# Optimization experiments

Hardware: AMD Instinct MI355X
Metric: run time of the kernel (lower is better)

Reference implementation:

```python
import jax, jax.numpy as jnp
import numpy as np

D_MODEL = 1024
N_HEADS = 16
D_K = D_MODEL // N_HEADS
ROPE_THETA = 10000.0


def setup_inputs() -> dict:
    key = jax.random.key(0)
    ks = jax.random.split(key, 5)
    B, S = 2, 2048
    std = (2.0 / (D_MODEL + D_MODEL)) ** 0.5
    x = jax.random.normal(ks[0], (B, S, D_MODEL), dtype=jnp.float32)
    Wq = jax.random.normal(ks[1], (D_MODEL, D_MODEL), dtype=jnp.float32) * std
    Wk = jax.random.normal(ks[2], (D_MODEL, D_MODEL), dtype=jnp.float32) * std
    Wv = jax.random.normal(ks[3], (D_MODEL, D_MODEL), dtype=jnp.float32) * std
    Wo = jax.random.normal(ks[4], (D_MODEL, D_MODEL), dtype=jnp.float32) * std
    token_positions = jnp.arange(S, dtype=jnp.int64 if jax.config.jax_enable_x64 else jnp.int32)
    return {"x": x, "Wq": Wq, "Wk": Wk, "Wv": Wv, "Wo": Wo,
            "token_positions": token_positions}


def _apply_rope(t, token_positions):
    # t: [B, H, S, d_k]; token_positions: [S]
    inv_freq = 1.0 / (ROPE_THETA ** (jnp.arange(0, D_K, 2, dtype=jnp.float32) / D_K))  # [d_k/2]
    freqs = token_positions.astype(jnp.float32)[:, None] * inv_freq[None, :]  # [S, d_k/2]
    cos, sin = jnp.cos(freqs), jnp.sin(freqs)
    x1, x2 = t[..., ::2], t[..., 1::2]
    xr = x1 * cos - x2 * sin
    yr = x1 * sin + x2 * cos
    # interleave back to even/odd positions
    out = jnp.stack([xr, yr], axis=-1).reshape(t.shape)
    return out


def reference(x, Wq, Wk, Wv, Wo, token_positions):
    B, S, D = x.shape
    H, dk = N_HEADS, D_K
    # projections: weight is [d_out, d_in], applied as x @ W.T
    def proj_heads(W):
        y = jnp.einsum('bsd,ed->bse', x, W)
        return y.reshape(B, S, H, dk).transpose(0, 2, 1, 3)  # [B,H,S,dk]
    q = proj_heads(Wq)
    k = proj_heads(Wk)
    v = proj_heads(Wv)
    q = _apply_rope(q, token_positions)
    k = _apply_rope(k, token_positions)
    scores = jnp.einsum('bhqd,bhkd->bhqk', q, k) / jnp.sqrt(jnp.float32(dk))
    causal = jnp.tril(jnp.ones((S, S), dtype=bool))
    scores = jnp.where(causal, scores, -jnp.inf)
    attn = jax.nn.softmax(scores, axis=-1)
    out = jnp.einsum('bhqk,bhkd->bhqd', attn, v)  # [B,H,S,dk]
    out = out.transpose(0, 2, 1, 3).reshape(B, S, D)
    return jnp.einsum('bsd,ed->bse', out, Wo)
```

## Files before the change

### kernel.cpp

```cpp
#include <hip/hip_runtime.h>

typedef __bf16 bf16x8 __attribute__((ext_vector_type(8)));
typedef float f32x4 __attribute__((ext_vector_type(4)));
typedef unsigned short u16x8 __attribute__((ext_vector_type(8)));


__device__ __forceinline__ unsigned short f2bf(float f) {
  unsigned u = __builtin_bit_cast(unsigned, f);
  u = (u + 0x7FFFu + ((u >> 16) & 1u)) >> 16;
  return (unsigned short)u;
}

__device__ __forceinline__ unsigned cvt_pk_bf16(float lo, float hi) {
  unsigned r;
  asm("v_cvt_pk_bf16_f32 %0, %1, %2" : "=v"(r) : "v"(lo), "v"(hi));
  return r;
}

__device__ __forceinline__ void load_lds16(const void* g, void* l) {
  __builtin_amdgcn_global_load_lds(
      (__attribute__((address_space(1))) void*)g,
      (__attribute__((address_space(3))) void*)l, 16, 0, 0);
}

__global__ __launch_bounds__(256) void k_convert(
    const float* __restrict__ x,
    const float* __restrict__ wq, const float* __restrict__ wk,
    const float* __restrict__ wv, const float* __restrict__ wo,
    unsigned short* __restrict__ xb,
    unsigned short* __restrict__ wqb, unsigned short* __restrict__ wkb,
    unsigned short* __restrict__ wvb, unsigned short* __restrict__ wob) {
  const int g = blockIdx.x * 256 + threadIdx.x;
  const float* src;
  unsigned short* dst;
  int off;
  if (g < (1 << 20)) {
    src = x; dst = xb; off = g;
  } else {
    const int q = g - (1 << 20);
    const int t = q >> 18;
    off = q & ((1 << 18) - 1);
    src = (t == 0) ? wq : (t == 1) ? wk : (t == 2) ? wv : wo;
    dst = (t == 0) ? wqb : (t == 1) ? wkb : (t == 2) ? wvb : wob;
  }
  const float4 v = ((const float4*)src)[off];
  ushort4 r;
  r.x = f2bf(v.x); r.y = f2bf(v.y); r.z = f2bf(v.z); r.w = f2bf(v.w);
  ((ushort4*)dst)[off] = r;
}

__global__ __launch_bounds__(256) void k_rope_tab(const int* __restrict__ tpos,
                                                  float* __restrict__ ct,
                                                  float* __restrict__ st) {
  const int idx = blockIdx.x * 256 + threadIdx.x;
  const int s = idx >> 5, i = idx & 31;
  const double p = (double)tpos[s];
  const double f = p * pow(10000.0, -(double)(2 * i) / 64.0);
  ct[idx] = (float)cos(f);
  st[idx] = (float)sin(f);
}

__device__ __forceinline__ void gemm_core_1024(
    const unsigned short* __restrict__ Ag,
    const unsigned short* __restrict__ Bg,
    unsigned short* As, unsigned short* Bs, f32x4 (&acc)[4][4], int tid) {
  const int lane = tid & 63;
  const int w = tid >> 6;
  const int wm = (w >> 1) * 64;
  const int wn = (w & 1) * 64;
  const int lr = lane & 15;
  const int lg8 = (lane >> 4) * 8;
  const int c0 = tid, c1 = 256 + tid;
  const int ar0 = c0 >> 2, ac0 = (c0 & 3) * 8;
  const int ar1 = c1 >> 2, ac1 = (c1 & 3) * 8;

  auto stage = [&](int buf, int kt) {
    unsigned short* Ab = As + buf * 4096;
    unsigned short* Bb = Bs + buf * 4096;
    load_lds16(Ag + ar0 * 1024 + kt + ac0, Ab + c0 * 8);
    load_lds16(Ag + ar1 * 1024 + kt + ac1, Ab + c1 * 8);
    load_lds16(Bg + ar0 * 1024 + kt + ac0, Bb + c0 * 8);
    load_lds16(Bg + ar1 * 1024 + kt + ac1, Bb + c1 * 8);
  };

  stage(0, 0);
  stage(1, 32);
  int cur = 0;
  for (int ki = 0; ki < 32; ++ki) {
    if (ki + 2 < 32) {
      int nb = cur + 2; if (nb >= 3) nb -= 3;
      stage(nb, (ki + 2) * 32);
      asm volatile("s_waitcnt vmcnt(8)" ::: "memory");
    } else if (ki + 1 < 32) {
      asm volatile("s_waitcnt vmcnt(4)" ::: "memory");
    } else {
      asm volatile("s_waitcnt vmcnt(0)" ::: "memory");
    }
    __builtin_amdgcn_s_barrier();
    const unsigned short* Ab = As + cur * 4096;
    const unsigned short* Bb = Bs + cur * 4096;
    bf16x8 af[4], bfv[4];
#pragma unroll
    for (int mi = 0; mi < 4; ++mi)
      af[mi] = *(const bf16x8*)(Ab + (wm + mi * 16 + lr) * 32 + lg8);
#pragma unroll
    for (int ni = 0; ni < 4; ++ni)
      bfv[ni] = *(const bf16x8*)(Bb + (wn + ni * 16 + lr) * 32 + lg8);
    __builtin_amdgcn_s_setprio(1);
#pragma unroll
    for (int mi = 0; mi < 4; ++mi)
#pragma unroll
      for (int ni = 0; ni < 4; ++ni)
        acc[mi][ni] = __builtin_amdgcn_mfma_f32_16x16x32_bf16(
            af[mi], bfv[ni], acc[mi][ni], 0, 0, 0);
    __builtin_amdgcn_s_setprio(0);
    __builtin_amdgcn_s_barrier();
    ++cur; if (cur == 3) cur = 0;
  }
}

__device__ __forceinline__ void gemm_core_bm64(
    const unsigned short* __restrict__ Ag,
    const unsigned short* __restrict__ Bg,
    unsigned short* As, unsigned short* Bs, f32x4 (&acc)[2][4], int tid) {
  const int lane = tid & 63;
  const int w = tid >> 6;
  const int wm = (w >> 1) * 32;
  const int wn = (w & 1) * 64;
  const int lr = lane & 15;
  const int lg8 = (lane >> 4) * 8;
  const int ar = tid >> 2, ac = (tid & 3) * 8;
  const int c0 = tid, c1 = 256 + tid;
  const int br0 = c0 >> 2, bc0 = (c0 & 3) * 8;
  const int br1 = c1 >> 2, bc1 = (c1 & 3) * 8;

  auto stage = [&](int buf, int kt) {
    load_lds16(Ag + ar * 1024 + kt + ac, As + buf * 2048 + tid * 8);
    load_lds16(Bg + br0 * 1024 + kt + bc0, Bs + buf * 4096 + c0 * 8);
    load_lds16(Bg + br1 * 1024 + kt + bc1, Bs + buf * 4096 + c1 * 8);
  };

  stage(0, 0);
  stage(1, 32);
  int cur = 0;
  for (int ki = 0; ki < 32; ++ki) {
    if (ki + 2 < 32) {
      int nb = cur + 2; if (nb >= 3) nb -= 3;
      stage(nb, (ki + 2) * 32);
      asm volatile("s_waitcnt vmcnt(6)" ::: "memory");
    } else if (ki + 1 < 32) {
      asm volatile("s_waitcnt vmcnt(3)" ::: "memory");
    } else {
      asm volatile("s_waitcnt vmcnt(0)" ::: "memory");
    }
    __builtin_amdgcn_s_barrier();
    const unsigned short* Ab = As + cur * 2048;
    const unsigned short* Bb = Bs + cur * 4096;
    bf16x8 af[2], bfv[4];
#pragma unroll
    for (int mi = 0; mi < 2; ++mi)
      af[mi] = *(const bf16x8*)(Ab + (wm + mi * 16 + lr) * 32 + lg8);
#pragma unroll
    for (int ni = 0; ni < 4; ++ni)
      bfv[ni] = *(const bf16x8*)(Bb + (wn + ni * 16 + lr) * 32 + lg8);
    __builtin_amdgcn_s_setprio(1);
#pragma unroll
    for (int mi = 0; mi < 2; ++mi)
#pragma unroll
      for (int ni = 0; ni < 4; ++ni)
        acc[mi][ni] = __builtin_amdgcn_mfma_f32_16x16x32_bf16(
            af[mi], bfv[ni], acc[mi][ni], 0, 0, 0);
    __builtin_amdgcn_s_setprio(0);
    __builtin_amdgcn_s_barrier();
    ++cur; if (cur == 3) cur = 0;
  }
}

__global__ __launch_bounds__(256) void k_proj(
    const unsigned short* __restrict__ Xb,
    const unsigned short* __restrict__ Wq, const unsigned short* __restrict__ Wk,
    const unsigned short* __restrict__ Wv,
    const float* __restrict__ ctab, const float* __restrict__ stab,
    unsigned short* __restrict__ Qo, unsigned short* __restrict__ Ko,
    unsigned short* __restrict__ Vo) {
  __shared__ __align__(16) unsigned short As[3 * 128 * 32];
  __shared__ __align__(16) unsigned short Bs[3 * 128 * 32];
  const int z = blockIdx.z;
  const unsigned short* Wsel = (z == 0) ? Wq : (z == 1) ? Wk : Wv;
  unsigned short* Out = (z == 0) ? Qo : (z == 1) ? Ko : Vo;
  const int tid = threadIdx.x;
  const int bm = blockIdx.x * 128, bn = blockIdx.y * 128;
  f32x4 acc[4][4] = {};
  gemm_core_1024(Xb + (size_t)bm * 1024, Wsel + (size_t)bn * 1024, As, Bs, acc, tid);

  const int lane = tid & 63, w = tid >> 6;
  const int wm = (w >> 1) * 64, wn = (w & 1) * 64;
  const int lr = lane & 15, lg = lane >> 4;

  if (z == 2) {
#pragma unroll
    for (int mi = 0; mi < 4; ++mi) {
      const int r0 = bm + wm + mi * 16 + lg * 4;
      const int s = r0 & 2047, b = r0 >> 11;
#pragma unroll
      for (int ni = 0; ni < 4; ++ni) {
        const int e = bn + wn + ni * 16 + lr;
        const int h = e >> 6, d = e & 63;
        ushort4 pk;
        pk.x = f2bf(acc[mi][ni][0]);
        pk.y = f2bf(acc[mi][ni][1]);
        pk.z = f2bf(acc[mi][ni][2]);
        pk.w = f2bf(acc[mi][ni][3]);
        *(ushort4*)&Out[((size_t)(b * 16 + h) * 64 + d) * 2048 + s] = pk;
      }
    }
    return;
  }

  const bool odd = lane & 1;
#pragma unroll
  for (int mi = 0; mi < 4; ++mi) {
#pragma unroll
    for (int ni = 0; ni < 4; ++ni) {
#pragma unroll
      for (int reg = 0; reg < 4; ++reg) {
        const int r = bm + wm + mi * 16 + lg * 4 + reg;
        const int e = bn + wn + ni * 16 + lr;
        float val = acc[mi][ni][reg];
        const float partner = __shfl_xor(val, 1);
        const int s = r & 2047, b = r >> 11;
        const int h = e >> 6, d = e & 63;
        const int i = d >> 1;
        const float c = ctab[s * 32 + i];
        const float sn = stab[s * 32 + i];
        const float outv = odd ? (val * c + partner * sn) : (val * c - partner * sn);
        Out[((size_t)(b * 16 + h) * 2048 + s) * 64 + d] = f2bf(outv);
      }
    }
  }
}

__global__ __launch_bounds__(64, 2) void k_attn(
    const unsigned short* __restrict__ Q, const unsigned short* __restrict__ K,
    const unsigned short* __restrict__ Vt, unsigned short* __restrict__ O) {
  __shared__ __align__(16) unsigned short Vs[2][64 * 64];
  __shared__ __align__(16) unsigned short Pl[16 * 68];
  const int L = blockIdx.x;
  const int bh = (L & 7) * 4 + ((L >> 3) & 3);
  const int p = L >> 5;
  const int qrowA = p * 16, qrowB = (127 - p) * 16;
  const int Ta = (qrowA + 79) >> 6;
  const int Tb = (qrowB + 79) >> 6;
  const int lane = threadIdx.x & 63;
  const int lr = lane & 15, lg = lane >> 4;
  const unsigned short* Qg = Q + (size_t)bh * 2048 * 64;
  const unsigned short* Kg = K + (size_t)bh * 2048 * 64;
  const unsigned short* Vg = Vt + (size_t)bh * 64 * 2048;

  bf16x8 qfA[2], qfB[2];
#pragma unroll
  for (int h = 0; h < 2; ++h) {
    qfA[h] = *(const bf16x8*)(Qg + (qrowA + lr) * 64 + h * 32 + lg * 8);
    qfB[h] = *(const bf16x8*)(Qg + (qrowB + lr) * 64 + h * 32 + lg * 8);
  }

  u16x8 ouv;
#pragma unroll
  for (int j = 0; j < 8; ++j) ouv[j] = 0x3F80;
  const bf16x8 onesf = __builtin_bit_cast(bf16x8, ouv);

  f32x4 oA[4] = {}, oB[4] = {};
  f32x4 lAa = {}, lBa = {};
  float mA = -__builtin_inff(), mB = -__builtin_inff();

  const float SCL = 0.125f * 1.44269504088896f;

  const int kbase = lr * 64 + lg * 8;
  const int vbase = (lane >> 3) * 2048 + (((lane & 7) ^ (lane >> 3)) * 8);

  auto loadK = [&](bf16x8 (&kd)[4][2], int kv) {
    const unsigned short* base = Kg + (size_t)kv * 4096 + kbase;
#pragma unroll
    for (int nt = 0; nt < 4; ++nt)
#pragma unroll
      for (int h = 0; h < 2; ++h)
        kd[nt][h] = *(const bf16x8*)(base + nt * 1024 + h * 32);
  };
  auto issueV = [&](int buf, int kv) {
    const unsigned short* src = Vg + kv * 64 + vbase;
    unsigned short* dst = &Vs[buf][0] + lane * 8;
#pragma unroll
    for (int i0 = 0; i0 < 8; ++i0)
      load_lds16(src + i0 * 16384, dst + i0 * 512);
  };

  auto soft = [&](f32x4 (&s)[4], float& m, f32x4& la, f32x4 (&oacc)[4],
                  int qrow, bool needmask, int kv) {
    if (needmask) {
      const int qg = qrow + lr;
#pragma unroll
      for (int nt = 0; nt < 4; ++nt)
#pragma unroll
        for (int reg = 0; reg < 4; ++reg) {
          const int kg = kv * 64 + nt * 16 + lg * 4 + reg;
          if (kg > qg) s[nt][reg] = -__builtin_inff();
        }
    }
    float t0 = fmaxf(fmaxf(s[0][0], s[0][1]), fmaxf(s[0][2], s[0][3]));
    float t1 = fmaxf(fmaxf(s[1][0], s[1][1]), fmaxf(s[1][2], s[1][3]));
    float t2 = fmaxf(fmaxf(s[2][0], s[2][1]), fmaxf(s[2][2], s[2][3]));
    float t3 = fmaxf(fmaxf(s[3][0], s[3][1]), fmaxf(s[3][2], s[3][3]));
    float pm = fmaxf(fmaxf(t0, t1), fmaxf(t2, t3));
    pm = fmaxf(pm, __shfl_xor(pm, 16));
    pm = fmaxf(pm, __shfl_xor(pm, 32));
    if (__any(pm > m)) {
      const float mn = fmaxf(m, pm);
      const float al = exp2f(SCL * (m - mn));
      m = mn;
#pragma unroll
      for (int reg = 0; reg < 4; ++reg) la[reg] *= al;
#pragma unroll
      for (int nt = 0; nt < 4; ++nt)
#pragma unroll
        for (int reg = 0; reg < 4; ++reg) oacc[nt][reg] *= al;
    }
    const float msc = SCL * m;
    unsigned short* prow = Pl + lr * 68;
#pragma unroll
    for (int nt = 0; nt < 4; ++nt) {
      const float p0 = exp2f(s[nt][0] * SCL - msc);
      const float p1 = exp2f(s[nt][1] * SCL - msc);
      const float p2 = exp2f(s[nt][2] * SCL - msc);
      const float p3 = exp2f(s[nt][3] * SCL - msc);
      const unsigned w01 = cvt_pk_bf16(p0, p1);
      const unsigned w23 = cvt_pk_bf16(p2, p3);
      ushort4 pk;
      pk.x = (unsigned short)w01; pk.y = (unsigned short)(w01 >> 16);
      pk.z = (unsigned short)w23; pk.w = (unsigned short)(w23 >> 16);
      *(ushort4*)(prow + nt * 16 + lg * 4) = pk;
    }
  };

  bf16x8 kbufA[4][2], kbufB[4][2];
  loadK(kbufA, 0);
  issueV(0, 0);

  auto iter = [&](int t, bf16x8 (&kc)[4][2], bf16x8 (&kn)[4][2]) {
    const bool more = (t + 1 < Tb);
    const bool actA = (t < Ta);
    if (more) { loadK(kn, t + 1); issueV((t + 1) & 1, t + 1); }

    f32x4 sB[4], sA[4];
    __builtin_amdgcn_s_setprio(1);
#pragma unroll
    for (int nt = 0; nt < 4; ++nt) {
      f32x4 z = {0.f, 0.f, 0.f, 0.f};
      z = __builtin_amdgcn_mfma_f32_16x16x32_bf16(kc[nt][0], qfB[0], z, 0, 0, 0);
      sB[nt] = __builtin_amdgcn_mfma_f32_16x16x32_bf16(kc[nt][1], qfB[1], z, 0, 0, 0);
    }
    if (actA)
#pragma unroll
      for (int nt = 0; nt < 4; ++nt) {
        f32x4 z = {0.f, 0.f, 0.f, 0.f};
        z = __builtin_amdgcn_mfma_f32_16x16x32_bf16(kc[nt][0], qfA[0], z, 0, 0, 0);
        sA[nt] = __builtin_amdgcn_mfma_f32_16x16x32_bf16(kc[nt][1], qfA[1], z, 0, 0, 0);
      }
    __builtin_amdgcn_s_setprio(0);

    soft(sB, mB, lBa, oB, qrowB, t == Tb - 1, t);
    bf16x8 paB[2], paA[2];
#pragma unroll
    for (int ks = 0; ks < 2; ++ks)
      paB[ks] = *(const bf16x8*)(Pl + lr * 68 + ks * 32 + lg * 8);
    if (actA) {
      soft(sA, mA, lAa, oA, qrowA, t == Ta - 1, t);
#pragma unroll
      for (int ks = 0; ks < 2; ++ks)
        paA[ks] = *(const bf16x8*)(Pl + lr * 68 + ks * 32 + lg * 8);
    }

    if (more) asm volatile("s_waitcnt vmcnt(16)" ::: "memory");
    else      asm volatile("s_waitcnt vmcnt(0)" ::: "memory");

    const unsigned short* Vw = &Vs[t & 1][0];
    __builtin_amdgcn_s_setprio(1);
    lBa = __builtin_amdgcn_mfma_f32_16x16x32_bf16(onesf, paB[0], lBa, 0, 0, 0);
    lBa = __builtin_amdgcn_mfma_f32_16x16x32_bf16(onesf, paB[1], lBa, 0, 0, 0);
    if (actA) {
      lAa = __builtin_amdgcn_mfma_f32_16x16x32_bf16(onesf, paA[0], lAa, 0, 0, 0);
      lAa = __builtin_amdgcn_mfma_f32_16x16x32_bf16(onesf, paA[1], lAa, 0, 0, 0);
    }
#pragma unroll
    for (int nt = 0; nt < 4; ++nt) {
      const int row = nt * 16 + lr;
      const bf16x8 vb0 = *(const bf16x8*)(Vw + row * 64 + ((lg ^ (row & 7)) * 8));
      const bf16x8 vb1 = *(const bf16x8*)(Vw + row * 64 + (((lg + 4) ^ (row & 7)) * 8));
      oB[nt] = __builtin_amdgcn_mfma_f32_16x16x32_bf16(vb0, paB[0], oB[nt], 0, 0, 0);
      oB[nt] = __builtin_amdgcn_mfma_f32_16x16x32_bf16(vb1, paB[1], oB[nt], 0, 0, 0);
      if (actA) {
        oA[nt] = __builtin_amdgcn_mfma_f32_16x16x32_bf16(vb0, paA[0], oA[nt], 0, 0, 0);
        oA[nt] = __builtin_amdgcn_mfma_f32_16x16x32_bf16(vb1, paA[1], oA[nt], 0, 0, 0);
      }
    }
    __builtin_amdgcn_s_setprio(0);
  };

  int t = 0;
  for (;;) {
    iter(t, kbufA, kbufB); ++t; if (t >= Tb) break;
    iter(t, kbufB, kbufA); ++t; if (t >= Tb) break;
  }

  const int b = bh >> 4, h = bh & 15;
  auto wrO = [&](f32x4 (&oacc)[4], float l, int qrow) {
    const float inv = 1.0f / l;
    unsigned short* dst = &O[((size_t)b * 2048 + qrow + lr) * 1024 + h * 64];
#pragma unroll
    for (int nt = 0; nt < 4; ++nt) {
      const unsigned w01 = cvt_pk_bf16(oacc[nt][0] * inv, oacc[nt][1] * inv);
      const unsigned w23 = cvt_pk_bf16(oacc[nt][2] * inv, oacc[nt][3] * inv);
      ushort4 pk;
      pk.x = (unsigned short)w01; pk.y = (unsigned short)(w01 >> 16);
      pk.z = (unsigned short)w23; pk.w = (unsigned short)(w23 >> 16);
      *(ushort4*)(dst + nt * 16 + lg * 4) = pk;
    }
  };
  wrO(oA, lAa[0], qrowA);
  wrO(oB, lBa[0], qrowB);
}

__global__ __launch_bounds__(256) void k_out(const unsigned short* __restrict__ Ab,
                                             const unsigned short* __restrict__ Wo,
                                             float* __restrict__ Out) {
  __shared__ __align__(16) unsigned short As[3 * 64 * 32];
  __shared__ __align__(16) unsigned short Bs[3 * 128 * 32];
  const int tid = threadIdx.x;
  const int bm = blockIdx.x * 64, bn = blockIdx.y * 128;
  f32x4 acc[2][4] = {};
  gemm_core_bm64(Ab + (size_t)bm * 1024, Wo + (size_t)bn * 1024, As, Bs, acc, tid);
  const int lane = tid & 63, w = tid >> 6;
  const int wm = (w >> 1) * 32, wn = (w & 1) * 64;
  const int lr = lane & 15, lg = lane >> 4;
#pragma unroll
  for (int mi = 0; mi < 2; ++mi)
#pragma unroll
    for (int ni = 0; ni < 4; ++ni)
#pragma unroll
      for (int reg = 0; reg < 4; ++reg) {
        const int r = bm + wm + mi * 16 + lg * 4 + reg;
        const int e = bn + wn + ni * 16 + lr;
        Out[(size_t)r * 1024 + e] = acc[mi][ni][reg];
      }
}

extern "C" void kernel_launch(void* const* d_in, const int* in_sizes, int n_in,
                              void* d_out, int out_size, void* d_ws, size_t ws_size,
                              hipStream_t stream) {
  const float* x = (const float*)d_in[0];
  const float* Wq = (const float*)d_in[1];
  const float* Wk = (const float*)d_in[2];
  const float* Wv = (const float*)d_in[3];
  const float* Wo = (const float*)d_in[4];
  const int* tpos = (const int*)d_in[5];
  float* out = (float*)d_out;
  char* ws = (char*)d_ws;
  const size_t MB = 1024 * 1024;
  unsigned short* xb = (unsigned short*)(ws);
  unsigned short* wqb = (unsigned short*)(ws + 8 * MB);
  unsigned short* wkb = (unsigned short*)(ws + 10 * MB);
  unsigned short* wvb = (unsigned short*)(ws + 12 * MB);
  unsigned short* wob = (unsigned short*)(ws + 14 * MB);
  unsigned short* Qb = (unsigned short*)(ws + 16 * MB);
  unsigned short* Kb = (unsigned short*)(ws + 24 * MB);
  unsigned short* Vtb = (unsigned short*)(ws + 32 * MB);
  unsigned short* Ab = (unsigned short*)(ws + 40 * MB);
  float* ctab = (float*)(ws + 48 * MB);
  float* stab = (float*)(ws + 48 * MB + 256 * 1024);

  k_convert<<<dim3(8192), dim3(256), 0, stream>>>(x, Wq, Wk, Wv, Wo, xb, wqb, wkb,
                                                  wvb, wob);
  k_rope_tab<<<dim3(256), dim3(256), 0, stream>>>(tpos, ctab, stab);
  k_proj<<<dim3(32, 8, 3), dim3(256), 0, stream>>>(xb, wqb, wkb, wvb, ctab, stab,
                                                   Qb, Kb, Vtb);
  k_attn<<<dim3(2048), dim3(64), 0, stream>>>(Qb, Kb, Vtb, Ab);
  k_out<<<dim3(64, 8), dim3(256), 0, stream>>>(Ab, wob, out);
}
```

Before: 151.3 us.

## Split long causal attention rows across KV halves and merge partials

The attention kernel stops pairing a short and a long query tile per block. Each block now handles one 16-row query tile. For the 60 longest tiles per head, the KV range is split into two halves computed by separate blocks, which write unnormalized bf16 partial outputs plus (max, sum). A new merge kernel combines them. It also drops K register double-buffering and V LDS double-buffering in favour of single buffers with full waits, and raises occupancy to 4 waves per SIMD. The goal is better load balance and more parallelism across 6016 blocks. The cost is an extra launch, partial-output traffic, bf16 rounding of the partials, and the loss of load/compute overlap within a block.

```diff
diff --git a/kernel.cpp b/kernel.cpp
--- a/kernel.cpp
+++ b/kernel.cpp
@@ -9,6 +9,10 @@
   unsigned u = __builtin_bit_cast(unsigned, f);
   u = (u + 0x7FFFu + ((u >> 16) & 1u)) >> 16;
   return (unsigned short)u;
+}
+
+__device__ __forceinline__ float bf2f(unsigned short v) {
+  return __builtin_bit_cast(float, ((unsigned)v) << 16);
 }
 
 __device__ __forceinline__ unsigned cvt_pk_bf16(float lo, float hi) {
@@ -240,76 +244,98 @@
   }
 }
 
-__global__ __launch_bounds__(64, 2) void k_attn(
+__global__ __launch_bounds__(64, 4) void k_attn(
     const unsigned short* __restrict__ Q, const unsigned short* __restrict__ K,
-    const unsigned short* __restrict__ Vt, unsigned short* __restrict__ O) {
-  __shared__ __align__(16) unsigned short Vs[2][64 * 64];
-  __shared__ __align__(16) unsigned short Pl[16 * 68];
+    const unsigned short* __restrict__ Vt, unsigned short* __restrict__ O,
+    unsigned short* __restrict__ OpLo, unsigned short* __restrict__ OpHi,
+    float2* __restrict__ mlLo, float2* __restrict__ mlHi) {
+  __shared__ __align__(16) unsigned short Vs[64 * 64];
+  __shared__ __align__(16) unsigned short Pl[16 * 64];
   const int L = blockIdx.x;
-  const int bh = (L & 7) * 4 + ((L >> 3) & 3);
-  const int p = L >> 5;
-  const int qrowA = p * 16, qrowB = (127 - p) * 16;
-  const int Ta = (qrowA + 79) >> 6;
-  const int Tb = (qrowB + 79) >> 6;
+  const int i = L >> 3;
+  const int bh = (L & 7) * 4 + (i & 3);
+  const int c = i >> 2;
+  int s, k0, k1, mode;
+  if (c < 60) {
+    s = 127 - c; const int T = (s * 16 + 79) >> 6; k0 = T >> 1; k1 = T; mode = 2;
+  } else if (c < 120) {
+    s = 127 - (c - 60); const int T = (s * 16 + 79) >> 6; k0 = 0; k1 = T >> 1; mode = 1;
+  } else {
+    s = 187 - c; k0 = 0; k1 = (s * 16 + 79) >> 6; mode = 0;
+  }
+  const int qrow = s * 16;
+  const bool masklast = (mode != 1);
   const int lane = threadIdx.x & 63;
   const int lr = lane & 15, lg = lane >> 4;
   const unsigned short* Qg = Q + (size_t)bh * 2048 * 64;
   const unsigned short* Kg = K + (size_t)bh * 2048 * 64;
   const unsigned short* Vg = Vt + (size_t)bh * 64 * 2048;
 
-  bf16x8 qfA[2], qfB[2];
-#pragma unroll
-  for (int h = 0; h < 2; ++h) {
-    qfA[h] = *(const bf16x8*)(Qg + (qrowA + lr) * 64 + h * 32 + lg * 8);
-    qfB[h] = *(const bf16x8*)(Qg + (qrowB + lr) * 64 + h * 32 + lg * 8);
-  }
+  bf16x8 qf[2];
+#pragma unroll
+  for (int h = 0; h < 2; ++h)
+    qf[h] = *(const bf16x8*)(Qg + (qrow + lr) * 64 + h * 32 + lg * 8);
 
   u16x8 ouv;
 #pragma unroll
   for (int j = 0; j < 8; ++j) ouv[j] = 0x3F80;
   const bf16x8 onesf = __builtin_bit_cast(bf16x8, ouv);
 
-  f32x4 oA[4] = {}, oB[4] = {};
-  f32x4 lAa = {}, lBa = {};
-  float mA = -__builtin_inff(), mB = -__builtin_inff();
+  f32x4 oacc[4] = {};
+  f32x4 la = {};
+  float m = -__builtin_inff();
 
   const float SCL = 0.125f * 1.44269504088896f;
 
   const int kbase = lr * 64 + lg * 8;
   const int vbase = (lane >> 3) * 2048 + (((lane & 7) ^ (lane >> 3)) * 8);
-
-  auto loadK = [&](bf16x8 (&kd)[4][2], int kv) {
-    const unsigned short* base = Kg + (size_t)kv * 4096 + kbase;
-#pragma unroll
-    for (int nt = 0; nt < 4; ++nt)
-#pragma unroll
-      for (int h = 0; h < 2; ++h)
-        kd[nt][h] = *(const bf16x8*)(base + nt * 1024 + h * 32);
-  };
-  auto issueV = [&](int buf, int kv) {
+  const int psw = (lr & 7) << 3;
+
+  auto issueV = [&](int kv) {
     const unsigned short* src = Vg + kv * 64 + vbase;
-    unsigned short* dst = &Vs[buf][0] + lane * 8;
+    unsigned short* dst = &Vs[0] + lane * 8;
 #pragma unroll
     for (int i0 = 0; i0 < 8; ++i0)
       load_lds16(src + i0 * 16384, dst + i0 * 512);
   };
 
-  auto soft = [&](f32x4 (&s)[4], float& m, f32x4& la, f32x4 (&oacc)[4],
-                  int qrow, bool needmask, int kv) {
-    if (needmask) {
+  issueV(k0);
+  for (int t = k0; t < k1; ++t) {
+    bf16x8 kb[4][2];
+    {
+      const unsigned short* base = Kg + (size_t)t * 4096 + kbase;
+#pragma unroll
+      for (int nt = 0; nt < 4; ++nt)
+#pragma unroll
+        for (int h = 0; h < 2; ++h)
+          kb[nt][h] = *(const bf16x8*)(base + nt * 1024 + h * 32);
+    }
+
+    f32x4 sacc[4];
+    __builtin_amdgcn_s_setprio(1);
+#pragma unroll
+    for (int nt = 0; nt < 4; ++nt) {
+      f32x4 z = {0.f, 0.f, 0.f, 0.f};
+      z = __builtin_amdgcn_mfma_f32_16x16x32_bf16(kb[nt][0], qf[0], z, 0, 0, 0);
+      sacc[nt] = __builtin_amdgcn_mfma_f32_16x16x32_bf16(kb[nt][1], qf[1], z, 0, 0, 0);
+    }
+    __builtin_amdgcn_s_setprio(0);
+
+    if (masklast && t == k1 - 1) {
       const int qg = qrow + lr;
 #pragma unroll
       for (int nt = 0; nt < 4; ++nt)
 #pragma unroll
         for (int reg = 0; reg < 4; ++reg) {
-          const int kg = kv * 64 + nt * 16 + lg * 4 + reg;
-          if (kg > qg) s[nt][reg] = -__builtin_inff();
+          const int kg = t * 64 + nt * 16 + lg * 4 + reg;
+          if (kg > qg) sacc[nt][reg] = -__builtin_inff();
         }
     }
-    float t0 = fmaxf(fmaxf(s[0][0], s[0][1]), fmaxf(s[0][2], s[0][3]));
-    float t1 = fmaxf(fmaxf(s[1][0], s[1][1]), fmaxf(s[1][2], s[1][3]));
-    float t2 = fmaxf(fmaxf(s[2][0], s[2][1]), fmaxf(s[2][2], s[2][3]));
-    float t3 = fmaxf(fmaxf(s[3][0], s[3][1]), fmaxf(s[3][2], s[3][3]));
+
+    float t0 = fmaxf(fmaxf(sacc[0][0], sacc[0][1]), fmaxf(sacc[0][2], sacc[0][3]));
+    float t1 = fmaxf(fmaxf(sacc[1][0], sacc[1][1]), fmaxf(sacc[1][2], sacc[1][3]));
+    float t2 = fmaxf(fmaxf(sacc[2][0], sacc[2][1]), fmaxf(sacc[2][2], sacc[2][3]));
+    float t3 = fmaxf(fmaxf(sacc[3][0], sacc[3][1]), fmaxf(sacc[3][2], sacc[3][3]));
     float pm = fmaxf(fmaxf(t0, t1), fmaxf(t2, t3));
     pm = fmaxf(pm, __shfl_xor(pm, 16));
     pm = fmaxf(pm, __shfl_xor(pm, 32));
@@ -325,95 +351,47 @@
         for (int reg = 0; reg < 4; ++reg) oacc[nt][reg] *= al;
     }
     const float msc = SCL * m;
-    unsigned short* prow = Pl + lr * 68;
+
 #pragma unroll
     for (int nt = 0; nt < 4; ++nt) {
-      const float p0 = exp2f(s[nt][0] * SCL - msc);
-      const float p1 = exp2f(s[nt][1] * SCL - msc);
-      const float p2 = exp2f(s[nt][2] * SCL - msc);
-      const float p3 = exp2f(s[nt][3] * SCL - msc);
+      const float p0 = exp2f(sacc[nt][0] * SCL - msc);
+      const float p1 = exp2f(sacc[nt][1] * SCL - msc);
+      const float p2 = exp2f(sacc[nt][2] * SCL - msc);
+      const float p3 = exp2f(sacc[nt][3] * SCL - msc);
       const unsigned w01 = cvt_pk_bf16(p0, p1);
       const unsigned w23 = cvt_pk_bf16(p2, p3);
       ushort4 pk;
       pk.x = (unsigned short)w01; pk.y = (unsigned short)(w01 >> 16);
       pk.z = (unsigned short)w23; pk.w = (unsigned short)(w23 >> 16);
-      *(ushort4*)(prow + nt * 16 + lg * 4) = pk;
-    }
-  };
-
-  bf16x8 kbufA[4][2], kbufB[4][2];
-  loadK(kbufA, 0);
-  issueV(0, 0);
-
-  auto iter = [&](int t, bf16x8 (&kc)[4][2], bf16x8 (&kn)[4][2]) {
-    const bool more = (t + 1 < Tb);
-    const bool actA = (t < Ta);
-    if (more) { loadK(kn, t + 1); issueV((t + 1) & 1, t + 1); }
-
-    f32x4 sB[4], sA[4];
+      *(ushort4*)(Pl + lr * 64 + ((nt * 16 + lg * 4) ^ psw)) = pk;
+    }
+    bf16x8 pa[2];
+#pragma unroll
+    for (int ks = 0; ks < 2; ++ks)
+      pa[ks] = *(const bf16x8*)(Pl + lr * 64 + ((ks * 32 + lg * 8) ^ psw));
+
+    asm volatile("s_waitcnt vmcnt(0)" ::: "memory");
+
     __builtin_amdgcn_s_setprio(1);
-#pragma unroll
-    for (int nt = 0; nt < 4; ++nt) {
-      f32x4 z = {0.f, 0.f, 0.f, 0.f};
-      z = __builtin_amdgcn_mfma_f32_16x16x32_bf16(kc[nt][0], qfB[0], z, 0, 0, 0);
-      sB[nt] = __builtin_amdgcn_mfma_f32_16x16x32_bf16(kc[nt][1], qfB[1], z, 0, 0, 0);
-    }
-    if (actA)
-#pragma unroll
-      for (int nt = 0; nt < 4; ++nt) {
-        f32x4 z = {0.f, 0.f, 0.f, 0.f};
-        z = __builtin_amdgcn_mfma_f32_16x16x32_bf16(kc[nt][0], qfA[0], z, 0, 0, 0);
-        sA[nt] = __builtin_amdgcn_mfma_f32_16x16x32_bf16(kc[nt][1], qfA[1], z, 0, 0, 0);
-      }
-    __builtin_amdgcn_s_setprio(0);
-
-    soft(sB, mB, lBa, oB, qrowB, t == Tb - 1, t);
-    bf16x8 paB[2], paA[2];
-#pragma unroll
-    for (int ks = 0; ks < 2; ++ks)
-      paB[ks] = *(const bf16x8*)(Pl + lr * 68 + ks * 32 + lg * 8);
-    if (actA) {
-      soft(sA, mA, lAa, oA, qrowA, t == Ta - 1, t);
-#pragma unroll
-      for (int ks = 0; ks < 2; ++ks)
-        paA[ks] = *(const bf16x8*)(Pl + lr * 68 + ks * 32 + lg * 8);
-    }
-
-    if (more) asm volatile("s_waitcnt vmcnt(16)" ::: "memory");
-    else      asm volatile("s_waitcnt vmcnt(0)" ::: "memory");
-
-    const unsigned short* Vw = &Vs[t & 1][0];
-    __builtin_amdgcn_s_setprio(1);
-    lBa = __builtin_amdgcn_mfma_f32_16x16x32_bf16(onesf, paB[0], lBa, 0, 0, 0);
-    lBa = __builtin_amdgcn_mfma_f32_16x16x32_bf16(onesf, paB[1], lBa, 0, 0, 0);
-    if (actA) {
-      lAa = __builtin_amdgcn_mfma_f32_16x16x32_bf16(onesf, paA[0], lAa, 0, 0, 0);
-      lAa = __builtin_amdgcn_mfma_f32_16x16x32_bf16(onesf, paA[1], lAa, 0, 0, 0);
-    }
+    la = __builtin_amdgcn_mfma_f32_16x16x32_bf16(onesf, pa[0], la, 0, 0, 0);
+    la = __builtin_amdgcn_mfma_f32_16x16x32_bf16(onesf, pa[1], la, 0, 0, 0);
 #pragma unroll
     for (int nt = 0; nt < 4; ++nt) {
       const int row = nt * 16 + lr;
-      const bf16x8 vb0 = *(const bf16x8*)(Vw + row * 64 + ((lg ^ (row & 7)) * 8));
-      const bf16x8 vb1 = *(const bf16x8*)(Vw + row * 64 + (((lg + 4) ^ (row & 7)) * 8));
-      oB[nt] = __builtin_amdgcn_mfma_f32_16x16x32_bf16(vb0, paB[0], oB[nt], 0, 0, 0);
-      oB[nt] = __builtin_amdgcn_mfma_f32_16x16x32_bf16(vb1, paB[1], oB[nt], 0, 0, 0);
-      if (actA) {
-        oA[nt] = __builtin_amdgcn_mfma_f32_16x16x32_bf16(vb0, paA[0], oA[nt], 0, 0, 0);
-        oA[nt] = __builtin_amdgcn_mfma_f32_16x16x32_bf16(vb1, paA[1], oA[nt], 0, 0, 0);
-      }
+      const bf16x8 vb0 = *(const bf16x8*)(Vs + row * 64 + ((lg ^ (row & 7)) * 8));
+      const bf16x8 vb1 = *(const bf16x8*)(Vs + row * 64 + (((lg + 4) ^ (row & 7)) * 8));
+      oacc[nt] = __builtin_amdgcn_mfma_f32_16x16x32_bf16(vb0, pa[0], oacc[nt], 0, 0, 0);
+      oacc[nt] = __builtin_amdgcn_mfma_f32_16x16x32_bf16(vb1, pa[1], oacc[nt], 0, 0, 0);
     }
     __builtin_amdgcn_s_setprio(0);
-  };
-
-  int t = 0;
-  for (;;) {
-    iter(t, kbufA, kbufB); ++t; if (t >= Tb) break;
-    iter(t, kbufB, kbufA); ++t; if (t >= Tb) break;
+
+    asm volatile("s_waitcnt lgkmcnt(0)" ::: "memory");
+    if (t + 1 < k1) issueV(t + 1);
   }
 
   const int b = bh >> 4, h = bh & 15;
-  auto wrO = [&](f32x4 (&oacc)[4], float l, int qrow) {
-    const float inv = 1.0f / l;
+  if (mode == 0) {
+    const float inv = 1.0f / la[0];
     unsigned short* dst = &O[((size_t)b * 2048 + qrow + lr) * 1024 + h * 64];
 #pragma unroll
     for (int nt = 0; nt < 4; ++nt) {
@@ -424,9 +402,60 @@
       pk.z = (unsigned short)w23; pk.w = (unsigned short)(w23 >> 16);
       *(ushort4*)(dst + nt * 16 + lg * 4) = pk;
     }
-  };
-  wrO(oA, lAa[0], qrowA);
-  wrO(oB, lBa[0], qrowB);
+  } else {
+    const int idx = bh * 60 + (s - 68);
+    unsigned short* dst = (mode == 1 ? OpLo : OpHi) + idx * 1024 + lr * 64;
+#pragma unroll
+    for (int nt = 0; nt < 4; ++nt) {
+      const unsigned w01 = cvt_pk_bf16(oacc[nt][0], oacc[nt][1]);
+      const unsigned w23 = cvt_pk_bf16(oacc[nt][2], oacc[nt][3]);
+      ushort4 pk;
+      pk.x = (unsigned short)w01; pk.y = (unsigned short)(w01 >> 16);
+      pk.z = (unsigned short)w23; pk.w = (unsigned short)(w23 >> 16);
+      *(ushort4*)(dst + nt * 16 + lg * 4) = pk;
+    }
+    if (lane < 16)
+      (mode == 1 ? mlLo : mlHi)[idx * 16 + lr] = make_float2(m, la[0]);
+  }
+}
+
+__global__ __launch_bounds__(256) void k_merge(
+    const unsigned short* __restrict__ OpLo, const unsigned short* __restrict__ OpHi,
+    const float2* __restrict__ mlLo, const float2* __restrict__ mlHi,
+    unsigned short* __restrict__ O) {
+  const int g = blockIdx.x * 4 + (threadIdx.x >> 6);
+  const int lane = threadIdx.x & 63;
+  const int bh = g / 60, sr = g - bh * 60;
+  const int s = 68 + sr;
+  const int q = lane & 15, dblk = lane >> 4;
+  const float SCL = 0.125f * 1.44269504088896f;
+  const float2 a = mlLo[g * 16 + q];
+  const float2 bm = mlHi[g * 16 + q];
+  const float mm = fmaxf(a.x, bm.x);
+  const float wl = exp2f(SCL * (a.x - mm));
+  const float wh = exp2f(SCL * (bm.x - mm));
+  const float inv = 1.0f / (a.y * wl + bm.y * wh);
+  const int off = g * 1024 + q * 64 + dblk * 16;
+  const u16x8 lo0 = *(const u16x8*)(OpLo + off);
+  const u16x8 lo1 = *(const u16x8*)(OpLo + off + 8);
+  const u16x8 hi0 = *(const u16x8*)(OpHi + off);
+  const u16x8 hi1 = *(const u16x8*)(OpHi + off + 8);
+  const int b = bh >> 4, h = bh & 15;
+  unsigned short* dst = &O[((size_t)b * 2048 + s * 16 + q) * 1024 + h * 64 + dblk * 16];
+  u16x8 r0, r1;
+#pragma unroll
+  for (int j = 0; j < 8; j += 2) {
+    const float f0 = (bf2f(lo0[j]) * wl + bf2f(hi0[j]) * wh) * inv;
+    const float f1 = (bf2f(lo0[j + 1]) * wl + bf2f(hi0[j + 1]) * wh) * inv;
+    const unsigned wpk = cvt_pk_bf16(f0, f1);
+    r0[j] = (unsigned short)wpk; r0[j + 1] = (unsigned short)(wpk >> 16);
+    const float g0 = (bf2f(lo1[j]) * wl + bf2f(hi1[j]) * wh) * inv;
+    const float g1 = (bf2f(lo1[j + 1]) * wl + bf2f(hi1[j + 1]) * wh) * inv;
+    const unsigned wpk2 = cvt_pk_bf16(g0, g1);
+    r1[j] = (unsigned short)wpk2; r1[j + 1] = (unsigned short)(wpk2 >> 16);
+  }
+  *(u16x8*)dst = r0;
+  *(u16x8*)(dst + 8) = r1;
 }
 
 __global__ __launch_bounds__(256) void k_out(const unsigned short* __restrict__ Ab,
@@ -476,12 +505,18 @@
   unsigned short* Ab = (unsigned short*)(ws + 40 * MB);
   float* ctab = (float*)(ws + 48 * MB);
   float* stab = (float*)(ws + 48 * MB + 256 * 1024);
+  unsigned short* OpLo = (unsigned short*)(ws);
+  unsigned short* OpHi = (unsigned short*)(ws + 4 * MB);
+  float2* mlLo = (float2*)(ws + 8 * MB);
+  float2* mlHi = (float2*)(ws + 9 * MB);
 
   k_convert<<<dim3(8192), dim3(256), 0, stream>>>(x, Wq, Wk, Wv, Wo, xb, wqb, wkb,
                                                   wvb, wob);
   k_rope_tab<<<dim3(256), dim3(256), 0, stream>>>(tpos, ctab, stab);
   k_proj<<<dim3(32, 8, 3), dim3(256), 0, stream>>>(xb, wqb, wkb, wvb, ctab, stab,
                                                    Qb, Kb, Vtb);
-  k_attn<<<dim3(2048), dim3(64), 0, stream>>>(Qb, Kb, Vtb, Ab);
+  k_attn<<<dim3(6016), dim3(64), 0, stream>>>(Qb, Kb, Vtb, Ab, OpLo, OpHi, mlLo,
+                                              mlHi);
+  k_merge<<<dim3(480), dim3(256), 0, stream>>>(OpLo, OpHi, mlLo, mlHi, Ab);
   k_out<<<dim3(64, 8), dim3(256), 0, stream>>>(Ab, wob, out);
 }
```

New measurement: 174.0 us. 1.15x slower.
